# Optimization experiments

Measured on AMD Instinct MI355X. Metric: run time of the kernel, lower is better.

## Reference

```python
import jax, jax.numpy as jnp
import numpy as np

N1, N2, N3, N4, D = 50000, 100000, 200000, 300000, 256


def setup_inputs() -> dict:
    key = jax.random.key(0)
    ks = jax.random.split(key, 10)
    feat = jax.random.normal(ks[0], (N1, D), dtype=jnp.float32) * 0.5  # scaled so level-4 products stay bounded
    c2a = jax.random.randint(ks[1], (N2,), 0, N1)
    c2b = jax.random.randint(ks[2], (N2,), 0, N1)
    c3a = jax.random.randint(ks[3], (N3,), 0, N2)
    c3b = jax.random.randint(ks[4], (N3,), 0, N2)
    c4a = jax.random.randint(ks[5], (N4,), 0, N3)
    c4b = jax.random.randint(ks[6], (N4,), 0, N3)
    W = jax.random.normal(ks[7], (D, D), dtype=jnp.float32) / jnp.sqrt(jnp.float32(D))
    b = jax.random.normal(ks[8], (D,), dtype=jnp.float32) * 0.01
    return {"feat": feat, "c2a": c2a, "c2b": c2b, "c3a": c3a, "c3b": c3b,
            "c4a": c4a, "c4b": c4b, "W": W, "b": b}


def _scatter_sum(h_parent, ca, cb, num_children):
    # each parent sends its feature to both children; children sum incoming messages
    z = jnp.zeros((num_children, h_parent.shape[1]), dtype=h_parent.dtype)
    return z.at[ca].add(h_parent).at[cb].add(h_parent)


def reference(feat, c2a, c2b, c3a, c3b, c4a, c4b, W, b):
    # upward: prod reduction over the two constituent subpaths (mailbox prod, dim=1)
    h1 = feat
    h2 = h1[c2a] * h1[c2b]            # [N2, D]
    h3 = h2[c3a] * h2[c3b]            # [N3, D]
    h4 = h3[c4a] * h3[c4b]            # [N4, D]
    # downward: sum-scatter parent -> children, h = h + h_down
    h3 = h3 + _scatter_sum(h4, c4a, c4b, h3.shape[0])
    h2 = h2 + _scatter_sum(h3, c3a, c3b, h2.shape[0])
    h1 = h1 + _scatter_sum(h2, c2a, c2b, h1.shape[0])
    # apply_nodes on n1: Linear + SiLU
    out = jax.nn.silu(h1 @ W + b)
    return out
```

## Files before the change

### kernel.cpp

```cpp
#include <hip/hip_runtime.h>
#include <cstdint>
#include <cstddef>

#define DD 256
#define DH 128
#define SCAN_BLK 256
#define SCAN_ELEMS 2048

__device__ __forceinline__ float2 mul2(float2 a, float2 b) {
    return make_float2(a.x * b.x, a.y * b.y);
}
__device__ __forceinline__ float2 add2(float2 a, float2 b) {
    return make_float2(a.x + b.x, a.y + b.y);
}
__device__ __forceinline__ float2 ldh(const float* __restrict__ base, int row, int lane) {
    return ((const float2*)(base + (size_t)row * DH))[lane];
}
__device__ __forceinline__ float2 ldf(const float* __restrict__ base, int row, int doff, int lane) {
    return ((const float2*)(base + (size_t)row * DD + doff))[lane];
}

__global__ void k_count_all(const int* __restrict__ c2a, const int* __restrict__ c2b,
                            const int* __restrict__ c3a, const int* __restrict__ c3b,
                            const int* __restrict__ c4a, const int* __restrict__ c4b,
                            int n2, int n3, int n4,
                            int* __restrict__ cnt4, int* __restrict__ cnt3,
                            int* __restrict__ cnt2) {
    int e = blockIdx.x * blockDim.x + threadIdx.x;
    if (e < n4) { atomicAdd(&cnt4[c4a[e]], 1); atomicAdd(&cnt4[c4b[e]], 1); }
    if (e < n3) { atomicAdd(&cnt3[c3a[e]], 1); atomicAdd(&cnt3[c3b[e]], 1); }
    if (e < n2) { atomicAdd(&cnt2[c2a[e]], 1); atomicAdd(&cnt2[c2b[e]], 1); }
}

__global__ void k_fill_all(const int* __restrict__ c2a, const int* __restrict__ c2b,
                           const int* __restrict__ c3a, const int* __restrict__ c3b,
                           const int* __restrict__ c4a, const int* __restrict__ c4b,
                           int n2, int n3, int n4,
                           int* __restrict__ cur4, int* __restrict__ cur3,
                           int* __restrict__ cur2,
                           int2* __restrict__ entp, int* __restrict__ ent3,
                           int* __restrict__ ent2,
                           int* __restrict__ pos3, int* __restrict__ pos2) {
    int e = blockIdx.x * blockDim.x + threadIdx.x;
    if (e < n4) {
        int a = c4a[e], b = c4b[e];
        int2 prA = make_int2(c3a[b], c3b[b]);
        int2 prB = make_int2(c3a[a], c3b[a]);
        int pa = atomicAdd(&cur4[a], 1);
        int pb = atomicAdd(&cur4[b], 1);
        entp[pa] = prA;
        entp[pb] = prB;
    }
    if (e < n3) {
        int a = c3a[e], b = c3b[e];
        int pa = atomicAdd(&cur3[a], 1);
        int pb = atomicAdd(&cur3[b], 1);
        ent3[pa] = e;
        ent3[pb] = e;
        pos3[2 * e] = pa;
        pos3[2 * e + 1] = pb;
    }
    if (e < n2) {
        int a = c2a[e], b = c2b[e];
        int pa = atomicAdd(&cur2[a], 1);
        int pb = atomicAdd(&cur2[b], 1);
        ent2[pa] = e;
        ent2[pb] = e;
        pos2[2 * e] = pa;
        pos2[2 * e + 1] = pb;
    }
}

__global__ void k_block_sums(const int* __restrict__ cnt, int n, int* __restrict__ bsum) {
    __shared__ int sdata[SCAN_BLK];
    int base = blockIdx.x * SCAN_ELEMS;
    int s = 0;
#pragma unroll
    for (int k = 0; k < 8; ++k) {
        int idx = base + threadIdx.x + k * SCAN_BLK;
        if (idx < n) s += cnt[idx];
    }
    sdata[threadIdx.x] = s;
    __syncthreads();
    for (int off = SCAN_BLK / 2; off > 0; off >>= 1) {
        if (threadIdx.x < off) sdata[threadIdx.x] += sdata[threadIdx.x + off];
        __syncthreads();
    }
    if (threadIdx.x == 0) bsum[blockIdx.x] = sdata[0];
}

__global__ void k_scan_bsums(int* __restrict__ bsum, int nb, int* __restrict__ total_out) {
    if (threadIdx.x == 0 && blockIdx.x == 0) {
        int acc = 0;
        for (int b = 0; b < nb; ++b) { int v = bsum[b]; bsum[b] = acc; acc += v; }
        *total_out = acc;
    }
}

__global__ void k_scan_final(const int* __restrict__ cnt, int n,
                             const int* __restrict__ bsum, int* __restrict__ offs,
                             int* __restrict__ cursor) {
    __shared__ int sdata[SCAN_BLK];
    int base = blockIdx.x * SCAN_ELEMS;
    int t0 = base + threadIdx.x * 8;
    int loc[8];
    int s = 0;
#pragma unroll
    for (int k = 0; k < 8; ++k) {
        int idx = t0 + k;
        int v = (idx < n) ? cnt[idx] : 0;
        loc[k] = s;
        s += v;
    }
    sdata[threadIdx.x] = s;
    __syncthreads();
    int run = s;
    for (int off = 1; off < SCAN_BLK; off <<= 1) {
        int add = (threadIdx.x >= (unsigned)off) ? sdata[threadIdx.x - off] : 0;
        __syncthreads();
        run += add;
        sdata[threadIdx.x] = run;
        __syncthreads();
    }
    int texcl = run - s + bsum[blockIdx.x];
#pragma unroll
    for (int k = 0; k < 8; ++k) {
        int idx = t0 + k;
        if (idx < n) {
            int v = texcl + loc[k];
            offs[idx] = v;
            cursor[idx] = v;
        }
    }
}

__global__ void k_h2_half(const float* __restrict__ feat, const int* __restrict__ c2a,
                          const int* __restrict__ c2b, float* __restrict__ h2h,
                          int n2, int doff) {
    int q = blockIdx.x * 4 + (threadIdx.x >> 6);
    int lane = threadIdx.x & 63;
    if (q >= n2) return;
    float2 v = mul2(ldf(feat, c2a[q], doff, lane), ldf(feat, c2b[q], doff, lane));
    ((float2*)(h2h + (size_t)q * DH))[lane] = v;
}

__global__ void k_h3tot_slot(const float* __restrict__ h2h,
                             const int* __restrict__ c3a, const int* __restrict__ c3b,
                             const int* __restrict__ offs4, const int2* __restrict__ entp,
                             const int* __restrict__ pos3, float* __restrict__ S3,
                             int n3) {
    int j = blockIdx.x * 4 + (threadIdx.x >> 6);
    int lane = threadIdx.x & 63;
    if (j >= n3) return;
    float2 own = mul2(ldh(h2h, c3a[j], lane), ldh(h2h, c3b[j], lane));
    float2 s = make_float2(0.f, 0.f);
    int e0 = offs4[j], e1 = offs4[j + 1];
    int e = e0;
    for (; e + 1 < e1; e += 2) {
        int2 p0 = entp[e], p1 = entp[e + 1];
        float2 a0 = ldh(h2h, p0.x, lane), b0 = ldh(h2h, p0.y, lane);
        float2 a1 = ldh(h2h, p1.x, lane), b1 = ldh(h2h, p1.y, lane);
        s = add2(s, add2(mul2(a0, b0), mul2(a1, b1)));
    }
    if (e < e1) {
        int2 p = entp[e];
        s = add2(s, mul2(ldh(h2h, p.x, lane), ldh(h2h, p.y, lane)));
    }
    float2 r = mul2(own, make_float2(1.f + s.x, 1.f + s.y));
    int s0 = pos3[2 * j], s1 = pos3[2 * j + 1];
    ((float2*)(S3 + (size_t)s0 * DH))[lane] = r;
    ((float2*)(S3 + (size_t)s1 * DH))[lane] = r;
}

__global__ void k_h3tot_half(const float* __restrict__ h2h,
                             const int* __restrict__ c3a, const int* __restrict__ c3b,
                             const int* __restrict__ offs4, const int2* __restrict__ entp,
                             float* __restrict__ h3th, int lo, int hi) {
    int j = lo + blockIdx.x * 4 + (threadIdx.x >> 6);
    int lane = threadIdx.x & 63;
    if (j >= hi) return;
    float2 own = mul2(ldh(h2h, c3a[j], lane), ldh(h2h, c3b[j], lane));
    float2 s = make_float2(0.f, 0.f);
    int e0 = offs4[j], e1 = offs4[j + 1];
    int e = e0;
    for (; e + 1 < e1; e += 2) {
        int2 p0 = entp[e], p1 = entp[e + 1];
        float2 a0 = ldh(h2h, p0.x, lane), b0 = ldh(h2h, p0.y, lane);
        float2 a1 = ldh(h2h, p1.x, lane), b1 = ldh(h2h, p1.y, lane);
        s = add2(s, add2(mul2(a0, b0), mul2(a1, b1)));
    }
    if (e < e1) {
        int2 p = entp[e];
        s = add2(s, mul2(ldh(h2h, p.x, lane), ldh(h2h, p.y, lane)));
    }
    float2 r = mul2(own, make_float2(1.f + s.x, 1.f + s.y));
    ((float2*)(h3th + (size_t)(j - lo) * DH))[lane] = r;
}

__global__ void k_m2_stream_inplace(float* __restrict__ h2h,
                                    const int* __restrict__ offs3,
                                    const float* __restrict__ S3, int n2) {
    int q = blockIdx.x * 4 + (threadIdx.x >> 6);
    int lane = threadIdx.x & 63;
    if (q >= n2) return;
    float2 h = ldh(h2h, q, lane);
    int f0 = offs3[q], f1 = offs3[q + 1];
    int f = f0;
    for (; f + 1 < f1; f += 2) {
        h = add2(h, add2(ldh(S3, f, lane), ldh(S3, f + 1, lane)));
    }
    if (f < f1) h = add2(h, ldh(S3, f, lane));
    ((float2*)(h2h + (size_t)q * DH))[lane] = h;
}

__global__ void k_m2_stream_slots(const float* __restrict__ h2h,
                                  const int* __restrict__ offs3,
                                  const float* __restrict__ S3,
                                  const int* __restrict__ pos2,
                                  float* __restrict__ S2, int n2) {
    int q = blockIdx.x * 4 + (threadIdx.x >> 6);
    int lane = threadIdx.x & 63;
    if (q >= n2) return;
    float2 h = ldh(h2h, q, lane);
    int f0 = offs3[q], f1 = offs3[q + 1];
    int f = f0;
    for (; f + 1 < f1; f += 2) {
        h = add2(h, add2(ldh(S3, f, lane), ldh(S3, f + 1, lane)));
    }
    if (f < f1) h = add2(h, ldh(S3, f, lane));
    int s0 = pos2[2 * q], s1 = pos2[2 * q + 1];
    ((float2*)(S2 + (size_t)s0 * DH))[lane] = h;
    ((float2*)(S2 + (size_t)s1 * DH))[lane] = h;
}

__global__ void k_m2_half(const float* __restrict__ h2h,
                          const int* __restrict__ offs3, const int* __restrict__ ent3,
                          const float* __restrict__ h3th, float* __restrict__ dst,
                          int n2, int lo, int hi, int first) {
    int q = blockIdx.x * 4 + (threadIdx.x >> 6);
    int lane = threadIdx.x & 63;
    if (q >= n2) return;
    float2 h = first ? ldh(h2h, q, lane) : ldh(dst, q, lane);
    int f0 = offs3[q], f1 = offs3[q + 1];
    int f = f0;
    for (; f + 1 < f1; f += 2) {
        int j0 = ent3[f], j1 = ent3[f + 1];
        bool in0 = (j0 >= lo) && (j0 < hi);
        bool in1 = (j1 >= lo) && (j1 < hi);
        if (in0 && in1) {
            h = add2(h, add2(ldh(h3th, j0 - lo, lane), ldh(h3th, j1 - lo, lane)));
        } else if (in0) {
            h = add2(h, ldh(h3th, j0 - lo, lane));
        } else if (in1) {
            h = add2(h, ldh(h3th, j1 - lo, lane));
        }
    }
    if (f < f1) {
        int j0 = ent3[f];
        if (j0 >= lo && j0 < hi) h = add2(h, ldh(h3th, j0 - lo, lane));
    }
    ((float2*)(dst + (size_t)q * DH))[lane] = h;
}

__global__ void k_h1_stream(const float* __restrict__ feat,
                            const int* __restrict__ offs2,
                            const float* __restrict__ S2,
                            float* __restrict__ out, int n1, int doff) {
    int i = blockIdx.x * 4 + (threadIdx.x >> 6);
    int lane = threadIdx.x & 63;
    if (i >= n1) return;
    float2 h = ldf(feat, i, doff, lane);
    int e0 = offs2[i], e1 = offs2[i + 1];
    int e = e0;
    for (; e + 1 < e1; e += 2) {
        h = add2(h, add2(ldh(S2, e, lane), ldh(S2, e + 1, lane)));
    }
    if (e < e1) h = add2(h, ldh(S2, e, lane));
    ((float2*)(out + (size_t)i * DD + doff))[lane] = h;
}

__global__ void k_h1_half(const float* __restrict__ feat, const float* __restrict__ m2,
                          const int* __restrict__ offs2, const int* __restrict__ ent2,
                          float* __restrict__ out, int n1, int doff) {
    int i = blockIdx.x * 4 + (threadIdx.x >> 6);
    int lane = threadIdx.x & 63;
    if (i >= n1) return;
    float2 h = ldf(feat, i, doff, lane);
    int e0 = offs2[i], e1 = offs2[i + 1];
    int e = e0;
    for (; e + 1 < e1; e += 2) {
        int q0 = ent2[e], q1 = ent2[e + 1];
        h = add2(h, add2(ldh(m2, q0, lane), ldh(m2, q1, lane)));
    }
    if (e < e1) h = add2(h, ldh(m2, ent2[e], lane));
    ((float2*)(out + (size_t)i * DD + doff))[lane] = h;
}

__device__ __forceinline__ float silu_f(float x) { return x / (1.0f + expf(-x)); }

__global__ __launch_bounds__(256) void k_gemm_silu(float* __restrict__ h,
                                                   const float* __restrict__ W,
                                                   const float* __restrict__ bias,
                                                   int n1) {
    __shared__ float As[32 * DD];
    const int t = threadIdx.x;
    const int row0 = blockIdx.x * 32;

    const float4* hv = (const float4*)h;
    float4* As4 = (float4*)As;
#pragma unroll
    for (int i = 0; i < 8; ++i) {
        int idx = t + i * 256;
        int r = idx >> 6, c = idx & 63;
        int gr = row0 + r;
        float4 v = make_float4(0.f, 0.f, 0.f, 0.f);
        if (gr < n1) v = hv[(size_t)gr * 64 + c];
        As4[idx] = v;
    }
    __syncthreads();

    const int rg = t >> 6;
    const int cg = t & 63;
    const float4* Wv = (const float4*)W;

    float4 acc[8];
#pragma unroll
    for (int r = 0; r < 8; ++r) acc[r] = make_float4(0.f, 0.f, 0.f, 0.f);

    for (int k = 0; k < DD; k += 4) {
        float4 a[8];
#pragma unroll
        for (int r = 0; r < 8; ++r)
            a[r] = *(const float4*)&As[(rg * 8 + r) * DD + k];
#pragma unroll
        for (int kk = 0; kk < 4; ++kk) {
            float4 w = Wv[(size_t)(k + kk) * 64 + cg];
#pragma unroll
            for (int r = 0; r < 8; ++r) {
                float av = (kk == 0) ? a[r].x : (kk == 1) ? a[r].y
                         : (kk == 2) ? a[r].z : a[r].w;
                acc[r].x += av * w.x;
                acc[r].y += av * w.y;
                acc[r].z += av * w.z;
                acc[r].w += av * w.w;
            }
        }
    }

    float4 bb = ((const float4*)bias)[cg];
    float4* ho = (float4*)h;
#pragma unroll
    for (int r = 0; r < 8; ++r) {
        int gr = row0 + rg * 8 + r;
        if (gr >= n1) continue;
        float4 x = acc[r];
        x.x = silu_f(x.x + bb.x);
        x.y = silu_f(x.y + bb.y);
        x.z = silu_f(x.z + bb.z);
        x.w = silu_f(x.w + bb.w);
        ho[(size_t)gr * 64 + cg] = x;
    }
}

static inline size_t al16(size_t x) { return (x + 15) & ~(size_t)15; }

extern "C" void kernel_launch(void* const* d_in, const int* in_sizes, int n_in,
                              void* d_out, int out_size, void* d_ws, size_t ws_size,
                              hipStream_t stream) {
    const float* feat = (const float*)d_in[0];
    const int* c2a = (const int*)d_in[1];
    const int* c2b = (const int*)d_in[2];
    const int* c3a = (const int*)d_in[3];
    const int* c3b = (const int*)d_in[4];
    const int* c4a = (const int*)d_in[5];
    const int* c4b = (const int*)d_in[6];
    const float* W = (const float*)d_in[7];
    const float* bias = (const float*)d_in[8];

    const int N1 = in_sizes[0] / DD;
    const int N2 = in_sizes[1];
    const int N3 = in_sizes[3];
    const int N4 = in_sizes[5];
    float* out = (float*)d_out;
    char* ws = (char*)d_ws;

    dim3 blk(256);
    auto rows_grid4 = [](int n) { return dim3((unsigned)((n + 3) / 4)); };
    auto thr_grid = [](int n) { return dim3((unsigned)((n + 255) / 256)); };

    size_t cnt4_b  = al16((size_t)N3 * 4);
    size_t cnt3_b  = al16((size_t)N2 * 4);
    size_t cnt2_b  = al16((size_t)N1 * 4);
    size_t cur4_b  = al16((size_t)N3 * 4);
    size_t cur3_b  = al16((size_t)N2 * 4);
    size_t cur2_b  = al16((size_t)N1 * 4);
    size_t bsum_b  = al16(4096);
    size_t offs4_b = al16((size_t)(N3 + 1) * 4);
    size_t entp_b  = al16((size_t)2 * N4 * 8);
    size_t offs3_b = al16((size_t)(N2 + 1) * 4);
    size_t ent3_b  = al16((size_t)2 * N3 * 4);
    size_t offs2_b = al16((size_t)(N1 + 1) * 4);
    size_t ent2_b  = al16((size_t)2 * N2 * 4);
    size_t pos3_b  = al16((size_t)2 * N3 * 4);
    size_t pos2_b  = al16((size_t)2 * N2 * 4);
    size_t fixed_b = cnt4_b + cnt3_b + cnt2_b + cur4_b + cur3_b + cur2_b + bsum_b +
                     offs4_b + entp_b + offs3_b + ent3_b + offs2_b + ent2_b +
                     pos3_b + pos2_b;
    size_t h2h_b = (size_t)N2 * DH * sizeof(float);
    size_t h3th_b = (size_t)N3 * DH * sizeof(float);
    size_t S3_b  = (size_t)2 * N3 * DH * sizeof(float);
    size_t S2_b  = (size_t)2 * N2 * DH * sizeof(float);

    char* p = ws;
    int* cnt4  = (int*)p; p += cnt4_b;
    int* cnt3  = (int*)p; p += cnt3_b;
    int* cnt2  = (int*)p; p += cnt2_b;
    int* cur4  = (int*)p; p += cur4_b;
    int* cur3  = (int*)p; p += cur3_b;
    int* cur2  = (int*)p; p += cur2_b;
    int* bsum  = (int*)p; p += bsum_b;
    int* offs4 = (int*)p; p += offs4_b;
    int2* entp = (int2*)p; p += entp_b;
    int* offs3 = (int*)p; p += offs3_b;
    int* ent3  = (int*)p; p += ent3_b;
    int* offs2 = (int*)p; p += offs2_b;
    int* ent2  = (int*)p; p += ent2_b;
    int* pos3  = (int*)p; p += pos3_b;
    int* pos2  = (int*)p; p += pos2_b;
    float* h2h = (float*)p; p += h2h_b;
    char* dyn = p;

    const bool tierAp = (ws_size >= fixed_b + h2h_b + S3_b + S2_b);
    const bool tierA  = !tierAp && (ws_size >= fixed_b + h2h_b + S3_b);
    const bool tierB  = !tierAp && !tierA && (ws_size >= fixed_b + h2h_b + h3th_b);

    auto scan_offs = [&](int* cn, int nnode, int* offs, int* cursor) {
        int nb = (nnode + SCAN_ELEMS - 1) / SCAN_ELEMS;
        k_block_sums<<<dim3((unsigned)nb), dim3(SCAN_BLK), 0, stream>>>(cn, nnode, bsum);
        k_scan_bsums<<<dim3(1), dim3(64), 0, stream>>>(bsum, nb, offs + nnode);
        k_scan_final<<<dim3((unsigned)nb), dim3(SCAN_BLK), 0, stream>>>(cn, nnode, bsum,
                                                                        offs, cursor);
    };

    int maxE = N2 > N3 ? N2 : N3;
    if (N4 > maxE) maxE = N4;
    hipMemsetAsync(cnt4, 0, cnt4_b + cnt3_b + cnt2_b, stream);
    k_count_all<<<thr_grid(maxE), blk, 0, stream>>>(c2a, c2b, c3a, c3b, c4a, c4b,
                                                    N2, N3, N4, cnt4, cnt3, cnt2);
    scan_offs(cnt4, N3, offs4, cur4);
    scan_offs(cnt3, N2, offs3, cur3);
    scan_offs(cnt2, N1, offs2, cur2);
    k_fill_all<<<thr_grid(maxE), blk, 0, stream>>>(c2a, c2b, c3a, c3b, c4a, c4b,
                                                   N2, N3, N4, cur4, cur3, cur2,
                                                   entp, ent3, ent2, pos3, pos2);

    if (tierAp) {
        float* S3 = (float*)dyn;
        float* S2 = (float*)(dyn + S3_b);
        for (int doff = 0; doff < DD; doff += DH) {
            k_h2_half<<<rows_grid4(N2), blk, 0, stream>>>(feat, c2a, c2b, h2h, N2, doff);
            k_h3tot_slot<<<rows_grid4(N3), blk, 0, stream>>>(h2h, c3a, c3b, offs4, entp,
                                                             pos3, S3, N3);
            k_m2_stream_slots<<<rows_grid4(N2), blk, 0, stream>>>(h2h, offs3, S3,
                                                                  pos2, S2, N2);
            k_h1_stream<<<rows_grid4(N1), blk, 0, stream>>>(feat, offs2, S2, out, N1, doff);
        }
    } else if (tierA) {
        float* S3 = (float*)dyn;
        for (int doff = 0; doff < DD; doff += DH) {
            k_h2_half<<<rows_grid4(N2), blk, 0, stream>>>(feat, c2a, c2b, h2h, N2, doff);
            k_h3tot_slot<<<rows_grid4(N3), blk, 0, stream>>>(h2h, c3a, c3b, offs4, entp,
                                                             pos3, S3, N3);
            k_m2_stream_inplace<<<rows_grid4(N2), blk, 0, stream>>>(h2h, offs3, S3, N2);
            k_h1_half<<<rows_grid4(N1), blk, 0, stream>>>(feat, h2h, offs2, ent2,
                                                          out, N1, doff);
        }
    } else if (tierB) {
        float* h3th = (float*)dyn;
        for (int doff = 0; doff < DD; doff += DH) {
            k_h2_half<<<rows_grid4(N2), blk, 0, stream>>>(feat, c2a, c2b, h2h, N2, doff);
            k_h3tot_half<<<rows_grid4(N3), blk, 0, stream>>>(h2h, c3a, c3b, offs4, entp,
                                                             h3th, 0, N3);
            k_m2_half<<<rows_grid4(N2), blk, 0, stream>>>(h2h, offs3, ent3, h3th,
                                                          h2h, N2, 0, N3, 1);
            k_h1_half<<<rows_grid4(N1), blk, 0, stream>>>(feat, h2h, offs2, ent2,
                                                          out, N1, doff);
        }
    } else {
        float* m2h = (float*)dyn;
        float* h3th = (float*)(dyn + h2h_b);
        size_t free_b = (ws_size > fixed_b + 2 * h2h_b) ? ws_size - fixed_b - 2 * h2h_b : 0;
        int chunk_rows = (int)(free_b / ((size_t)DH * sizeof(float)));
        if (chunk_rows > N3) chunk_rows = N3;
        if (chunk_rows < 1) chunk_rows = 1;
        int C = (N3 + chunk_rows - 1) / chunk_rows;
        chunk_rows = (N3 + C - 1) / C;

        for (int doff = 0; doff < DD; doff += DH) {
            k_h2_half<<<rows_grid4(N2), blk, 0, stream>>>(feat, c2a, c2b, h2h, N2, doff);
            int first = 1;
            for (int lo = 0; lo < N3; lo += chunk_rows) {
                int hi = lo + chunk_rows;
                if (hi > N3) hi = N3;
                k_h3tot_half<<<rows_grid4(hi - lo), blk, 0, stream>>>(h2h, c3a, c3b,
                                                                      offs4, entp,
                                                                      h3th, lo, hi);
                k_m2_half<<<rows_grid4(N2), blk, 0, stream>>>(h2h, offs3, ent3, h3th,
                                                              m2h, N2, lo, hi, first);
                first = 0;
            }
            k_h1_half<<<rows_grid4(N1), blk, 0, stream>>>(feat, m2h, offs2, ent2,
                                                          out, N1, doff);
        }
    }

    k_gemm_silu<<<dim3((unsigned)((N1 + 31) / 32)), blk, 0, stream>>>(out, W, bias, N1);
}
```

Before: 778.0 us.

## Drop slot-scatter tiers, process two rows per wave, enlarge GEMM tile

Removes the S3/S2 slot-buffer paths and the pos3/pos2 arrays, so the default path now writes h3 totals once and gathers them through ent3. The level-3 and m2 kernels each handle two rows per wavefront with interleaved loops, which puts more independent gathers in flight. The GEMM tile grows from 32 to 64 rows per block, which raises register pressure. The chunked m2 loop is also simplified. The slot approach used contiguous streaming reads, so dropping it swaps those for random gathers while writing half as much.

```diff
diff --git a/kernel.cpp b/kernel.cpp
--- a/kernel.cpp
+++ b/kernel.cpp
@@ -39,8 +39,7 @@
                            int* __restrict__ cur4, int* __restrict__ cur3,
                            int* __restrict__ cur2,
                            int2* __restrict__ entp, int* __restrict__ ent3,
-                           int* __restrict__ ent2,
-                           int* __restrict__ pos3, int* __restrict__ pos2) {
+                           int* __restrict__ ent2) {
     int e = blockIdx.x * blockDim.x + threadIdx.x;
     if (e < n4) {
         int a = c4a[e], b = c4b[e];
@@ -57,8 +56,6 @@
         int pb = atomicAdd(&cur3[b], 1);
         ent3[pa] = e;
         ent3[pb] = e;
-        pos3[2 * e] = pa;
-        pos3[2 * e + 1] = pb;
     }
     if (e < n2) {
         int a = c2a[e], b = c2b[e];
@@ -66,8 +63,6 @@
         int pb = atomicAdd(&cur2[b], 1);
         ent2[pa] = e;
         ent2[pb] = e;
-        pos2[2 * e] = pa;
-        pos2[2 * e + 1] = pb;
     }
 }
 
@@ -144,32 +139,100 @@
     ((float2*)(h2h + (size_t)q * DH))[lane] = v;
 }
 
-__global__ void k_h3tot_slot(const float* __restrict__ h2h,
+__global__ void k_h3tot_dual(const float* __restrict__ h2h,
                              const int* __restrict__ c3a, const int* __restrict__ c3b,
                              const int* __restrict__ offs4, const int2* __restrict__ entp,
-                             const int* __restrict__ pos3, float* __restrict__ S3,
-                             int n3) {
-    int j = blockIdx.x * 4 + (threadIdx.x >> 6);
-    int lane = threadIdx.x & 63;
-    if (j >= n3) return;
-    float2 own = mul2(ldh(h2h, c3a[j], lane), ldh(h2h, c3b[j], lane));
-    float2 s = make_float2(0.f, 0.f);
-    int e0 = offs4[j], e1 = offs4[j + 1];
-    int e = e0;
-    for (; e + 1 < e1; e += 2) {
-        int2 p0 = entp[e], p1 = entp[e + 1];
-        float2 a0 = ldh(h2h, p0.x, lane), b0 = ldh(h2h, p0.y, lane);
-        float2 a1 = ldh(h2h, p1.x, lane), b1 = ldh(h2h, p1.y, lane);
-        s = add2(s, add2(mul2(a0, b0), mul2(a1, b1)));
-    }
-    if (e < e1) {
-        int2 p = entp[e];
-        s = add2(s, mul2(ldh(h2h, p.x, lane), ldh(h2h, p.y, lane)));
-    }
-    float2 r = mul2(own, make_float2(1.f + s.x, 1.f + s.y));
-    int s0 = pos3[2 * j], s1 = pos3[2 * j + 1];
-    ((float2*)(S3 + (size_t)s0 * DH))[lane] = r;
-    ((float2*)(S3 + (size_t)s1 * DH))[lane] = r;
+                             float* __restrict__ h3th, int n3) {
+    int w = blockIdx.x * 4 + (threadIdx.x >> 6);
+    int lane = threadIdx.x & 63;
+    int j0 = w * 2, j1 = j0 + 1;
+    if (j0 >= n3) return;
+    bool v1 = (j1 < n3);
+    float2 own0 = mul2(ldh(h2h, c3a[j0], lane), ldh(h2h, c3b[j0], lane));
+    float2 own1 = make_float2(0.f, 0.f);
+    int a1 = 0, b1 = 0;
+    if (v1) {
+        own1 = mul2(ldh(h2h, c3a[j1], lane), ldh(h2h, c3b[j1], lane));
+        a1 = offs4[j1]; b1 = offs4[j1 + 1];
+    }
+    int a0 = offs4[j0], b0 = offs4[j0 + 1];
+    float2 s0 = make_float2(0.f, 0.f), s1 = make_float2(0.f, 0.f);
+    while (a0 + 1 < b0 && a1 + 1 < b1) {
+        int2 p00 = entp[a0], p01 = entp[a0 + 1];
+        int2 p10 = entp[a1], p11 = entp[a1 + 1];
+        float2 x00a = ldh(h2h, p00.x, lane), x00b = ldh(h2h, p00.y, lane);
+        float2 x01a = ldh(h2h, p01.x, lane), x01b = ldh(h2h, p01.y, lane);
+        float2 x10a = ldh(h2h, p10.x, lane), x10b = ldh(h2h, p10.y, lane);
+        float2 x11a = ldh(h2h, p11.x, lane), x11b = ldh(h2h, p11.y, lane);
+        s0 = add2(s0, add2(mul2(x00a, x00b), mul2(x01a, x01b)));
+        s1 = add2(s1, add2(mul2(x10a, x10b), mul2(x11a, x11b)));
+        a0 += 2; a1 += 2;
+    }
+    for (; a0 + 1 < b0; a0 += 2) {
+        int2 p0 = entp[a0], p1 = entp[a0 + 1];
+        float2 xa = ldh(h2h, p0.x, lane), xb = ldh(h2h, p0.y, lane);
+        float2 ya = ldh(h2h, p1.x, lane), yb = ldh(h2h, p1.y, lane);
+        s0 = add2(s0, add2(mul2(xa, xb), mul2(ya, yb)));
+    }
+    if (a0 < b0) {
+        int2 p = entp[a0];
+        s0 = add2(s0, mul2(ldh(h2h, p.x, lane), ldh(h2h, p.y, lane)));
+    }
+    for (; a1 + 1 < b1; a1 += 2) {
+        int2 p0 = entp[a1], p1 = entp[a1 + 1];
+        float2 xa = ldh(h2h, p0.x, lane), xb = ldh(h2h, p0.y, lane);
+        float2 ya = ldh(h2h, p1.x, lane), yb = ldh(h2h, p1.y, lane);
+        s1 = add2(s1, add2(mul2(xa, xb), mul2(ya, yb)));
+    }
+    if (a1 < b1) {
+        int2 p = entp[a1];
+        s1 = add2(s1, mul2(ldh(h2h, p.x, lane), ldh(h2h, p.y, lane)));
+    }
+    float2 r0 = mul2(own0, make_float2(1.f + s0.x, 1.f + s0.y));
+    ((float2*)(h3th + (size_t)j0 * DH))[lane] = r0;
+    if (v1) {
+        float2 r1 = mul2(own1, make_float2(1.f + s1.x, 1.f + s1.y));
+        ((float2*)(h3th + (size_t)j1 * DH))[lane] = r1;
+    }
+}
+
+__global__ void k_m2_dual(float* __restrict__ h2h,
+                          const int* __restrict__ offs3, const int* __restrict__ ent3,
+                          const float* __restrict__ h3th, int n2) {
+    int w = blockIdx.x * 4 + (threadIdx.x >> 6);
+    int lane = threadIdx.x & 63;
+    int q0 = w * 2, q1 = q0 + 1;
+    if (q0 >= n2) return;
+    bool v1 = (q1 < n2);
+    float2 h0 = ldh(h2h, q0, lane);
+    float2 h1v = make_float2(0.f, 0.f);
+    int a1 = 0, b1 = 0;
+    if (v1) {
+        h1v = ldh(h2h, q1, lane);
+        a1 = offs3[q1]; b1 = offs3[q1 + 1];
+    }
+    int a0 = offs3[q0], b0 = offs3[q0 + 1];
+    while (a0 + 1 < b0 && a1 + 1 < b1) {
+        int j00 = ent3[a0], j01 = ent3[a0 + 1];
+        int j10 = ent3[a1], j11 = ent3[a1 + 1];
+        float2 x00 = ldh(h3th, j00, lane), x01 = ldh(h3th, j01, lane);
+        float2 x10 = ldh(h3th, j10, lane), x11 = ldh(h3th, j11, lane);
+        h0 = add2(h0, add2(x00, x01));
+        h1v = add2(h1v, add2(x10, x11));
+        a0 += 2; a1 += 2;
+    }
+    for (; a0 + 1 < b0; a0 += 2) {
+        float2 x0 = ldh(h3th, ent3[a0], lane), x1 = ldh(h3th, ent3[a0 + 1], lane);
+        h0 = add2(h0, add2(x0, x1));
+    }
+    if (a0 < b0) h0 = add2(h0, ldh(h3th, ent3[a0], lane));
+    for (; a1 + 1 < b1; a1 += 2) {
+        float2 x0 = ldh(h3th, ent3[a1], lane), x1 = ldh(h3th, ent3[a1 + 1], lane);
+        h1v = add2(h1v, add2(x0, x1));
+    }
+    if (a1 < b1) h1v = add2(h1v, ldh(h3th, ent3[a1], lane));
+    ((float2*)(h2h + (size_t)q0 * DH))[lane] = h0;
+    if (v1) ((float2*)(h2h + (size_t)q1 * DH))[lane] = h1v;
 }
 
 __global__ void k_h3tot_half(const float* __restrict__ h2h,
@@ -197,42 +260,6 @@
     ((float2*)(h3th + (size_t)(j - lo) * DH))[lane] = r;
 }
 
-__global__ void k_m2_stream_inplace(float* __restrict__ h2h,
-                                    const int* __restrict__ offs3,
-                                    const float* __restrict__ S3, int n2) {
-    int q = blockIdx.x * 4 + (threadIdx.x >> 6);
-    int lane = threadIdx.x & 63;
-    if (q >= n2) return;
-    float2 h = ldh(h2h, q, lane);
-    int f0 = offs3[q], f1 = offs3[q + 1];
-    int f = f0;
-    for (; f + 1 < f1; f += 2) {
-        h = add2(h, add2(ldh(S3, f, lane), ldh(S3, f + 1, lane)));
-    }
-    if (f < f1) h = add2(h, ldh(S3, f, lane));
-    ((float2*)(h2h + (size_t)q * DH))[lane] = h;
-}
-
-__global__ void k_m2_stream_slots(const float* __restrict__ h2h,
-                                  const int* __restrict__ offs3,
-                                  const float* __restrict__ S3,
-                                  const int* __restrict__ pos2,
-                                  float* __restrict__ S2, int n2) {
-    int q = blockIdx.x * 4 + (threadIdx.x >> 6);
-    int lane = threadIdx.x & 63;
-    if (q >= n2) return;
-    float2 h = ldh(h2h, q, lane);
-    int f0 = offs3[q], f1 = offs3[q + 1];
-    int f = f0;
-    for (; f + 1 < f1; f += 2) {
-        h = add2(h, add2(ldh(S3, f, lane), ldh(S3, f + 1, lane)));
-    }
-    if (f < f1) h = add2(h, ldh(S3, f, lane));
-    int s0 = pos2[2 * q], s1 = pos2[2 * q + 1];
-    ((float2*)(S2 + (size_t)s0 * DH))[lane] = h;
-    ((float2*)(S2 + (size_t)s1 * DH))[lane] = h;
-}
-
 __global__ void k_m2_half(const float* __restrict__ h2h,
                           const int* __restrict__ offs3, const int* __restrict__ ent3,
                           const float* __restrict__ h3th, float* __restrict__ dst,
@@ -242,41 +269,11 @@
     if (q >= n2) return;
     float2 h = first ? ldh(h2h, q, lane) : ldh(dst, q, lane);
     int f0 = offs3[q], f1 = offs3[q + 1];
-    int f = f0;
-    for (; f + 1 < f1; f += 2) {
-        int j0 = ent3[f], j1 = ent3[f + 1];
-        bool in0 = (j0 >= lo) && (j0 < hi);
-        bool in1 = (j1 >= lo) && (j1 < hi);
-        if (in0 && in1) {
-            h = add2(h, add2(ldh(h3th, j0 - lo, lane), ldh(h3th, j1 - lo, lane)));
-        } else if (in0) {
-            h = add2(h, ldh(h3th, j0 - lo, lane));
-        } else if (in1) {
-            h = add2(h, ldh(h3th, j1 - lo, lane));
-        }
-    }
-    if (f < f1) {
+    for (int f = f0; f < f1; ++f) {
         int j0 = ent3[f];
         if (j0 >= lo && j0 < hi) h = add2(h, ldh(h3th, j0 - lo, lane));
     }
     ((float2*)(dst + (size_t)q * DH))[lane] = h;
-}
-
-__global__ void k_h1_stream(const float* __restrict__ feat,
-                            const int* __restrict__ offs2,
-                            const float* __restrict__ S2,
-                            float* __restrict__ out, int n1, int doff) {
-    int i = blockIdx.x * 4 + (threadIdx.x >> 6);
-    int lane = threadIdx.x & 63;
-    if (i >= n1) return;
-    float2 h = ldf(feat, i, doff, lane);
-    int e0 = offs2[i], e1 = offs2[i + 1];
-    int e = e0;
-    for (; e + 1 < e1; e += 2) {
-        h = add2(h, add2(ldh(S2, e, lane), ldh(S2, e + 1, lane)));
-    }
-    if (e < e1) h = add2(h, ldh(S2, e, lane));
-    ((float2*)(out + (size_t)i * DD + doff))[lane] = h;
 }
 
 __global__ void k_h1_half(const float* __restrict__ feat, const float* __restrict__ m2,
@@ -298,18 +295,20 @@
 
 __device__ __forceinline__ float silu_f(float x) { return x / (1.0f + expf(-x)); }
 
+#define GEMM_ROWS 64
+
 __global__ __launch_bounds__(256) void k_gemm_silu(float* __restrict__ h,
                                                    const float* __restrict__ W,
                                                    const float* __restrict__ bias,
                                                    int n1) {
-    __shared__ float As[32 * DD];
+    __shared__ float As[GEMM_ROWS * DD];
     const int t = threadIdx.x;
-    const int row0 = blockIdx.x * 32;
+    const int row0 = blockIdx.x * GEMM_ROWS;
 
     const float4* hv = (const float4*)h;
     float4* As4 = (float4*)As;
 #pragma unroll
-    for (int i = 0; i < 8; ++i) {
+    for (int i = 0; i < 16; ++i) {
         int idx = t + i * 256;
         int r = idx >> 6, c = idx & 63;
         int gr = row0 + r;
@@ -323,20 +322,20 @@
     const int cg = t & 63;
     const float4* Wv = (const float4*)W;
 
-    float4 acc[8];
-#pragma unroll
-    for (int r = 0; r < 8; ++r) acc[r] = make_float4(0.f, 0.f, 0.f, 0.f);
+    float4 acc[16];
+#pragma unroll
+    for (int r = 0; r < 16; ++r) acc[r] = make_float4(0.f, 0.f, 0.f, 0.f);
 
     for (int k = 0; k < DD; k += 4) {
-        float4 a[8];
-#pragma unroll
-        for (int r = 0; r < 8; ++r)
-            a[r] = *(const float4*)&As[(rg * 8 + r) * DD + k];
+        float4 a[16];
+#pragma unroll
+        for (int r = 0; r < 16; ++r)
+            a[r] = *(const float4*)&As[(rg * 16 + r) * DD + k];
 #pragma unroll
         for (int kk = 0; kk < 4; ++kk) {
             float4 w = Wv[(size_t)(k + kk) * 64 + cg];
 #pragma unroll
-            for (int r = 0; r < 8; ++r) {
+            for (int r = 0; r < 16; ++r) {
                 float av = (kk == 0) ? a[r].x : (kk == 1) ? a[r].y
                          : (kk == 2) ? a[r].z : a[r].w;
                 acc[r].x += av * w.x;
@@ -350,8 +349,8 @@
     float4 bb = ((const float4*)bias)[cg];
     float4* ho = (float4*)h;
 #pragma unroll
-    for (int r = 0; r < 8; ++r) {
-        int gr = row0 + rg * 8 + r;
+    for (int r = 0; r < 16; ++r) {
+        int gr = row0 + rg * 16 + r;
         if (gr >= n1) continue;
         float4 x = acc[r];
         x.x = silu_f(x.x + bb.x);
@@ -386,6 +385,7 @@
 
     dim3 blk(256);
     auto rows_grid4 = [](int n) { return dim3((unsigned)((n + 3) / 4)); };
+    auto dual_grid = [](int n) { return dim3((unsigned)((n + 7) / 8)); };
     auto thr_grid = [](int n) { return dim3((unsigned)((n + 255) / 256)); };
 
     size_t cnt4_b  = al16((size_t)N3 * 4);
@@ -401,15 +401,10 @@
     size_t ent3_b  = al16((size_t)2 * N3 * 4);
     size_t offs2_b = al16((size_t)(N1 + 1) * 4);
     size_t ent2_b  = al16((size_t)2 * N2 * 4);
-    size_t pos3_b  = al16((size_t)2 * N3 * 4);
-    size_t pos2_b  = al16((size_t)2 * N2 * 4);
     size_t fixed_b = cnt4_b + cnt3_b + cnt2_b + cur4_b + cur3_b + cur2_b + bsum_b +
-                     offs4_b + entp_b + offs3_b + ent3_b + offs2_b + ent2_b +
-                     pos3_b + pos2_b;
+                     offs4_b + entp_b + offs3_b + ent3_b + offs2_b + ent2_b;
     size_t h2h_b = (size_t)N2 * DH * sizeof(float);
     size_t h3th_b = (size_t)N3 * DH * sizeof(float);
-    size_t S3_b  = (size_t)2 * N3 * DH * sizeof(float);
-    size_t S2_b  = (size_t)2 * N2 * DH * sizeof(float);
 
     char* p = ws;
     int* cnt4  = (int*)p; p += cnt4_b;
@@ -425,14 +420,10 @@
     int* ent3  = (int*)p; p += ent3_b;
     int* offs2 = (int*)p; p += offs2_b;
     int* ent2  = (int*)p; p += ent2_b;
-    int* pos3  = (int*)p; p += pos3_b;
-    int* pos2  = (int*)p; p += pos2_b;
     float* h2h = (float*)p; p += h2h_b;
     char* dyn = p;
 
-    const bool tierAp = (ws_size >= fixed_b + h2h_b + S3_b + S2_b);
-    const bool tierA  = !tierAp && (ws_size >= fixed_b + h2h_b + S3_b);
-    const bool tierB  = !tierAp && !tierA && (ws_size >= fixed_b + h2h_b + h3th_b);
+    const bool single = (ws_size >= fixed_b + h2h_b + h3th_b);
 
     auto scan_offs = [&](int* cn, int nnode, int* offs, int* cursor) {
         int nb = (nnode + SCAN_ELEMS - 1) / SCAN_ELEMS;
@@ -452,37 +443,15 @@
     scan_offs(cnt2, N1, offs2, cur2);
     k_fill_all<<<thr_grid(maxE), blk, 0, stream>>>(c2a, c2b, c3a, c3b, c4a, c4b,
                                                    N2, N3, N4, cur4, cur3, cur2,
-                                                   entp, ent3, ent2, pos3, pos2);
-
-    if (tierAp) {
-        float* S3 = (float*)dyn;
-        float* S2 = (float*)(dyn + S3_b);
-        for (int doff = 0; doff < DD; doff += DH) {
-            k_h2_half<<<rows_grid4(N2), blk, 0, stream>>>(feat, c2a, c2b, h2h, N2, doff);
-            k_h3tot_slot<<<rows_grid4(N3), blk, 0, stream>>>(h2h, c3a, c3b, offs4, entp,
-                                                             pos3, S3, N3);
-            k_m2_stream_slots<<<rows_grid4(N2), blk, 0, stream>>>(h2h, offs3, S3,
-                                                                  pos2, S2, N2);
-            k_h1_stream<<<rows_grid4(N1), blk, 0, stream>>>(feat, offs2, S2, out, N1, doff);
-        }
-    } else if (tierA) {
-        float* S3 = (float*)dyn;
-        for (int doff = 0; doff < DD; doff += DH) {
-            k_h2_half<<<rows_grid4(N2), blk, 0, stream>>>(feat, c2a, c2b, h2h, N2, doff);
-            k_h3tot_slot<<<rows_grid4(N3), blk, 0, stream>>>(h2h, c3a, c3b, offs4, entp,
-                                                             pos3, S3, N3);
-            k_m2_stream_inplace<<<rows_grid4(N2), blk, 0, stream>>>(h2h, offs3, S3, N2);
-            k_h1_half<<<rows_grid4(N1), blk, 0, stream>>>(feat, h2h, offs2, ent2,
-                                                          out, N1, doff);
-        }
-    } else if (tierB) {
+                                                   entp, ent3, ent2);
+
+    if (single) {
         float* h3th = (float*)dyn;
         for (int doff = 0; doff < DD; doff += DH) {
             k_h2_half<<<rows_grid4(N2), blk, 0, stream>>>(feat, c2a, c2b, h2h, N2, doff);
-            k_h3tot_half<<<rows_grid4(N3), blk, 0, stream>>>(h2h, c3a, c3b, offs4, entp,
-                                                             h3th, 0, N3);
-            k_m2_half<<<rows_grid4(N2), blk, 0, stream>>>(h2h, offs3, ent3, h3th,
-                                                          h2h, N2, 0, N3, 1);
+            k_h3tot_dual<<<dual_grid(N3), blk, 0, stream>>>(h2h, c3a, c3b, offs4, entp,
+                                                            h3th, N3);
+            k_m2_dual<<<dual_grid(N2), blk, 0, stream>>>(h2h, offs3, ent3, h3th, N2);
             k_h1_half<<<rows_grid4(N1), blk, 0, stream>>>(feat, h2h, offs2, ent2,
                                                           out, N1, doff);
         }
@@ -514,5 +483,6 @@
         }
     }
 
-    k_gemm_silu<<<dim3((unsigned)((N1 + 31) / 32)), blk, 0, stream>>>(out, W, bias, N1);
-}
+    k_gemm_silu<<<dim3((unsigned)((N1 + GEMM_ROWS - 1) / GEMM_ROWS)), blk, 0, stream>>>(
+        out, W, bias, N1);
+}
```

New measurement: 780.5 us. Within noise of the previous version (+0.3%).
